# Optimization experiments

Measured on AMD Instinct MI355X. Metric: run time of the kernel, lower is better.

## Reference

```python
import jax, jax.numpy as jnp
import numpy as np

DIM = 768
NUM_HEADS = 12
HEAD_DIM = DIM // NUM_HEADS
SCALE = HEAD_DIM ** -0.5


def setup_inputs() -> dict:
    key = jax.random.key(0)
    ks = jax.random.split(key, 7)
    B, N, C = 8, 1024, DIM
    x = jax.random.normal(ks[0], (B, N, C), dtype=jnp.float32)
    mask = jax.random.randint(ks[1], (B, N), 0, 2) > 0  # True = masked out
    qkv_w = jax.random.normal(ks[2], (3 * C, C), dtype=jnp.float32) * 0.02
    q_bias = jax.random.normal(ks[3], (C,), dtype=jnp.float32) * 0.02
    v_bias = jax.random.normal(ks[4], (C,), dtype=jnp.float32) * 0.02
    proj_w = jax.random.normal(ks[5], (C, C), dtype=jnp.float32) * 0.02
    proj_b = jax.random.normal(ks[6], (C,), dtype=jnp.float32) * 0.02
    return {"x": x, "mask": mask, "qkv_w": qkv_w, "q_bias": q_bias,
            "v_bias": v_bias, "proj_w": proj_w, "proj_b": proj_b}


def reference(x, mask, qkv_w, q_bias, v_bias, proj_w, proj_b):
    B, N, C = x.shape
    # CAE bias: concat(q_bias, zeros, v_bias) for the fused qkv projection
    qkv_bias = jnp.concatenate([q_bias, jnp.zeros_like(v_bias), v_bias])
    qkv = x @ qkv_w.T + qkv_bias  # [B, N, 3C]
    qkv = qkv.reshape(B, N, 3, NUM_HEADS, HEAD_DIM)
    q, k, v = (qkv[:, :, i].transpose(0, 2, 1, 3) for i in range(3))  # [B,H,N,hd]
    attn = jnp.einsum('bhqd,bhkd->bhqk', q * SCALE, k)  # [B,H,N,N]
    attn = jnp.where(mask[:, None, None, :], -jnp.inf, attn)
    attn = jax.nn.softmax(attn, axis=-1)
    out = jnp.einsum('bhqk,bhkd->bhqd', attn, v)  # [B,H,N,hd]
    out = out.transpose(0, 2, 1, 3).reshape(B, N, C)
    return out @ proj_w.T + proj_b
```

## Files before the change

### kernel.cpp

```cpp
#include <hip/hip_runtime.h>
#include <cstddef>
#include <cstdint>


typedef __attribute__((ext_vector_type(4))) float f32x4;
typedef __attribute__((ext_vector_type(8))) __bf16 bf16x8;
typedef __attribute__((ext_vector_type(4))) unsigned int uint4v;
typedef __attribute__((ext_vector_type(2))) unsigned int uint2v;
typedef __attribute__((ext_vector_type(4))) unsigned short ushort4v;

#define QK_PRESCALE 0.18033688011112042f

__device__ __forceinline__ unsigned short f2bf(float f) {
  return (unsigned short)((__float_as_uint(f) + 0x8000u) >> 16);
}
__device__ __forceinline__ unsigned int pack2bf(float flo, float fhi) {
  unsigned ulo = __float_as_uint(flo) + 0x8000u;
  unsigned uhi = __float_as_uint(fhi) + 0x8000u;
  return __builtin_amdgcn_perm(uhi, ulo, 0x07060302);
}

__device__ __forceinline__ void gl_lds16(const unsigned short* g, unsigned short* l) {
  __builtin_amdgcn_global_load_lds(
      (const __attribute__((address_space(1))) unsigned int*)g,
      (__attribute__((address_space(3))) unsigned int*)l, 16, 0, 0);
}

__global__ __launch_bounds__(256)
void cvt_kernel(const float* __restrict__ src, unsigned short* __restrict__ dst, int n4) {
  int i = blockIdx.x * 256 + threadIdx.x;
  if (i < n4) {
    float4 v = ((const float4*)src)[i];
    uint2v o;
    o.x = pack2bf(v.x, v.y);
    o.y = pack2bf(v.z, v.w);
    ((uint2v*)dst)[i] = o;
  }
}

__global__ __launch_bounds__(256)
void qkv_gemm(const unsigned short* __restrict__ xb, const unsigned short* __restrict__ wb,
              const float* __restrict__ qb, const float* __restrict__ vb,
              unsigned short* __restrict__ qo, unsigned short* __restrict__ ko,
              unsigned short* __restrict__ vto) {
  __shared__ __align__(16) unsigned short smem[17408];
  const int tid = threadIdx.x;
  const int lane = tid & 63, wid = tid >> 6;
  const int lm = lane & 15, lq = lane >> 4;
  const int wm = (wid & 1) * 64, wn = (wid >> 1) * 64;
  const int xsw = lm & 7;
  const int L = blockIdx.x;
  const int xcd = L & 7, s = L >> 3;
  const int m0 = (xcd * 8 + (s & 7)) * 128;
  const int n0 = (s >> 3) * 128;
  const bool sw = (n0 < 1536);
  const unsigned short* Ab = sw ? wb : xb;
  const unsigned short* Bb = sw ? xb : wb;
  const int Ao = sw ? n0 : m0;
  const int Bo = sw ? m0 : n0;
  const int srow = lane >> 3;
  const int scolsw = ((lane & 7) ^ srow) * 8;
  const unsigned short* ga = Ab + (size_t)(Ao + wid * 32 + srow) * 768 + scolsw;
  const unsigned short* gb = Bb + (size_t)(Bo + wid * 32 + srow) * 768 + scolsw;
  f32x4 acc[4][4] = {};

  for (int kt = 0; kt < 768; kt += 64) {
#pragma unroll
    for (int i = 0; i < 4; ++i) {
      gl_lds16(ga + kt + (size_t)i * 8 * 768, &smem[(wid * 32 + i * 8) * 64]);
      gl_lds16(gb + kt + (size_t)i * 8 * 768, &smem[8192 + (wid * 32 + i * 8) * 64]);
    }
    __syncthreads();
#pragma unroll
    for (int ks = 0; ks < 2; ++ks) {
      bf16x8 af[4], bf[4];
#pragma unroll
      for (int i = 0; i < 4; ++i)
        af[i] = *(const bf16x8*)&smem[(wm + i * 16 + lm) * 64 + (((ks * 4 + lq) ^ xsw) * 8)];
#pragma unroll
      for (int i = 0; i < 4; ++i)
        bf[i] = *(const bf16x8*)&smem[8192 + (wn + i * 16 + lm) * 64 + (((ks * 4 + lq) ^ xsw) * 8)];
#pragma unroll
      for (int mi = 0; mi < 4; ++mi)
#pragma unroll
        for (int ni = 0; ni < 4; ++ni)
          acc[mi][ni] = __builtin_amdgcn_mfma_f32_16x16x32_bf16(af[mi], bf[ni], acc[mi][ni], 0, 0, 0);
    }
    __syncthreads();
  }

  if (sw) {
    const int which = (n0 >= 768) ? 1 : 0;
    const int within0 = n0 - which * 768;
#pragma unroll
    for (int mi = 0; mi < 4; ++mi) {
      int d0 = wm + mi * 16 + lq * 4;
      f32x4 bias4 = {0.f, 0.f, 0.f, 0.f};
      if (which == 0) bias4 = *(const f32x4*)&qb[within0 + d0];
#pragma unroll
      for (int ni = 0; ni < 4; ++ni) {
        int tokl = wn + ni * 16 + lm;
        uint2v pk;
        if (which == 0) {
          pk.x = pack2bf((acc[mi][ni][0] + bias4[0]) * QK_PRESCALE,
                         (acc[mi][ni][1] + bias4[1]) * QK_PRESCALE);
          pk.y = pack2bf((acc[mi][ni][2] + bias4[2]) * QK_PRESCALE,
                         (acc[mi][ni][3] + bias4[3]) * QK_PRESCALE);
        } else {
          pk.x = pack2bf(acc[mi][ni][0], acc[mi][ni][1]);
          pk.y = pack2bf(acc[mi][ni][2], acc[mi][ni][3]);
        }
        *(uint2v*)&smem[tokl * 136 + d0] = pk;
      }
    }
    __syncthreads();
    {
      int tok = tid >> 1, half = tid & 1;
      int b = m0 >> 10;
      int tokg = (m0 & 1023) + tok;
      int hh = (within0 >> 6) + half;
      unsigned short* dst = which ? ko : qo;
      size_t base = (((size_t)(b * 12 + hh)) * 1024 + tokg) * 64;
      const unsigned short* srcr = &smem[tok * 136 + half * 64];
#pragma unroll
      for (int j = 0; j < 8; ++j)
        *(uint4v*)&dst[base + j * 8] = *(const uint4v*)&srcr[j * 8];
    }
  } else {
    const int within0 = n0 - 1536;
#pragma unroll
    for (int mi = 0; mi < 4; ++mi) {
      int tok0 = wm + mi * 16 + lq * 4;
#pragma unroll
      for (int ni = 0; ni < 4; ++ni) {
        int dl = wn + ni * 16 + lm;
        float bias = vb[within0 + dl];
        uint2v pk;
        pk.x = pack2bf(acc[mi][ni][0] + bias, acc[mi][ni][1] + bias);
        pk.y = pack2bf(acc[mi][ni][2] + bias, acc[mi][ni][3] + bias);
        *(uint2v*)&smem[dl * 136 + tok0] = pk;
      }
    }
    __syncthreads();
    {
      int dl = tid >> 1, halft = tid & 1;
      int within = within0 + dl;
      int hh = within >> 6, d = within & 63;
      int b = m0 >> 10;
      int tokg0 = (m0 & 1023) + halft * 64;
      size_t base = (((size_t)(b * 12 + hh)) * 64 + d) * 1024 + tokg0;
      const unsigned short* srcr = &smem[dl * 136 + halft * 64];
#pragma unroll
      for (int j = 0; j < 8; ++j)
        *(uint4v*)&vto[base + j * 8] = *(const uint4v*)&srcr[j * 8];
    }
  }
}

__global__ __launch_bounds__(256)
void attn_mfma(const unsigned short* __restrict__ q, const unsigned short* __restrict__ k,
               const unsigned short* __restrict__ vt, const int* __restrict__ mask,
               unsigned short* __restrict__ ao) {
  __shared__ unsigned short ks_s[64 * 64];
  __shared__ unsigned short vs_s[64 * 64];
  __shared__ unsigned short ps[4][32 * 72];
  __shared__ float mkl[64];
  const int tid = threadIdx.x;
  const int lane = tid & 63, wid = tid >> 6;
  const int lm = lane & 15, lq = lane >> 4;
  const int xsw = lm & 7;
  const int L = blockIdx.x;
  const int xcd = L & 7, s = L >> 3;
  const int bh = xcd * 12 + s / 8;
  const int qt = s % 8;
  const int bb = bh / 12, hh = bh % 12;
  const unsigned short* qp = q + (size_t)bh * 65536;
  const unsigned short* kp = k + (size_t)bh * 65536;
  const unsigned short* vp = vt + (size_t)bh * 65536;
  const int* mp = mask + bb * 1024;
  const int q0 = qt * 128 + wid * 32;
  const int srow = lane >> 3;
  const int scolsw = ((lane & 7) ^ srow) * 8;
  const unsigned short* gk = kp + (size_t)(wid * 16 + srow) * 64 + scolsw;
  const unsigned short* gv = vp + (size_t)(wid * 16 + srow) * 1024 + scolsw;

  bf16x8 qf[2][2];
#pragma unroll
  for (int mi = 0; mi < 2; ++mi)
#pragma unroll
    for (int ks2 = 0; ks2 < 2; ++ks2)
      qf[mi][ks2] = *(const bf16x8*)&qp[(size_t)(q0 + mi * 16 + lm) * 64 + ks2 * 32 + lq * 8];
  bf16x8 ones;
#pragma unroll
  for (int i = 0; i < 8; ++i) ones[i] = (__bf16)1.0f;

  f32x4 o_acc[2][4] = {};
  f32x4 l_acc[2] = {};

  for (int kt = 0; kt < 16; ++kt) {
    __syncthreads();
#pragma unroll
    for (int i = 0; i < 2; ++i) {
      gl_lds16(gk + (size_t)kt * 4096 + (size_t)i * 8 * 64, &ks_s[(wid * 16 + i * 8) * 64]);
      gl_lds16(gv + (size_t)kt * 64 + (size_t)i * 8 * 1024, &vs_s[(wid * 16 + i * 8) * 64]);
    }
    if (tid < 64) mkl[tid] = mp[kt * 64 + tid] ? -1e30f : 0.0f;
    __syncthreads();

    f32x4 st[4][2] = {};
#pragma unroll
    for (int ks2 = 0; ks2 < 2; ++ks2) {
      bf16x8 kf[4];
#pragma unroll
      for (int nt = 0; nt < 4; ++nt)
        kf[nt] = *(const bf16x8*)&ks_s[(nt * 16 + lm) * 64 + (((ks2 * 4 + lq) ^ xsw) * 8)];
#pragma unroll
      for (int nt = 0; nt < 4; ++nt)
#pragma unroll
        for (int mi = 0; mi < 2; ++mi)
          st[nt][mi] = __builtin_amdgcn_mfma_f32_16x16x32_bf16(kf[nt], qf[mi][ks2], st[nt][mi], 0, 0, 0);
    }

#pragma unroll
    for (int nt = 0; nt < 4; ++nt) {
      f32x4 mv4 = *(const f32x4*)&mkl[nt * 16 + lq * 4];
#pragma unroll
      for (int mi = 0; mi < 2; ++mi) {
        uint2v pk;
        pk.x = pack2bf(__builtin_amdgcn_exp2f(st[nt][mi][0] + mv4[0]),
                       __builtin_amdgcn_exp2f(st[nt][mi][1] + mv4[1]));
        pk.y = pack2bf(__builtin_amdgcn_exp2f(st[nt][mi][2] + mv4[2]),
                       __builtin_amdgcn_exp2f(st[nt][mi][3] + mv4[3]));
        *(uint2v*)&ps[wid][(mi * 16 + lm) * 72 + nt * 16 + lq * 4] = pk;
      }
    }

#pragma unroll
    for (int ks2 = 0; ks2 < 2; ++ks2) {
      bf16x8 pf[2], vf[4];
#pragma unroll
      for (int mi = 0; mi < 2; ++mi)
        pf[mi] = *(const bf16x8*)&ps[wid][(mi * 16 + lm) * 72 + ks2 * 32 + lq * 8];
#pragma unroll
      for (int nt = 0; nt < 4; ++nt)
        vf[nt] = *(const bf16x8*)&vs_s[(nt * 16 + lm) * 64 + (((ks2 * 4 + lq) ^ xsw) * 8)];
#pragma unroll
      for (int mi = 0; mi < 2; ++mi) {
#pragma unroll
        for (int nt = 0; nt < 4; ++nt)
          o_acc[mi][nt] = __builtin_amdgcn_mfma_f32_16x16x32_bf16(pf[mi], vf[nt], o_acc[mi][nt], 0, 0, 0);
        l_acc[mi] = __builtin_amdgcn_mfma_f32_16x16x32_bf16(pf[mi], ones, l_acc[mi], 0, 0, 0);
      }
    }
  }

#pragma unroll
  for (int mi = 0; mi < 2; ++mi) {
#pragma unroll
    for (int r = 0; r < 4; ++r) {
      float inv = 1.0f / l_acc[mi][r];
      int tok = q0 + mi * 16 + lq * 4 + r;
#pragma unroll
      for (int nt = 0; nt < 4; ++nt)
        ao[(size_t)(bb * 1024 + tok) * 768 + hh * 64 + nt * 16 + lm] = f2bf(o_acc[mi][nt][r] * inv);
    }
  }
}

__global__ __launch_bounds__(256)
void proj_gemm(const unsigned short* __restrict__ ab, const unsigned short* __restrict__ wb,
               const float* __restrict__ pb, float* __restrict__ out) {
  __shared__ unsigned short as[128 * 64];
  __shared__ unsigned short bs[128 * 64];
  const int tid = threadIdx.x;
  const int lane = tid & 63, wid = tid >> 6;
  const int lm = lane & 15, lq = lane >> 4;
  const int xsw = lm & 7;
  const int wm = (wid & 1) * 64, wn = (wid >> 1) * 64;
  const int L = blockIdx.x;
  const int xcd = L & 7, s = L >> 3;
  const int m0 = (xcd * 8 + s / 6) * 128;
  const int n0 = (s % 6) * 128;
  const int srow = lane >> 3;
  const int scolsw = ((lane & 7) ^ srow) * 8;
  const unsigned short* ga = wb + (size_t)(n0 + wid * 32 + srow) * 768 + scolsw;
  const unsigned short* gb = ab + (size_t)(m0 + wid * 32 + srow) * 768 + scolsw;
  f32x4 acc[4][4] = {};
  for (int kt = 0; kt < 768; kt += 64) {
#pragma unroll
    for (int i = 0; i < 4; ++i) {
      gl_lds16(ga + kt + (size_t)i * 8 * 768, &as[(wid * 32 + i * 8) * 64]);
      gl_lds16(gb + kt + (size_t)i * 8 * 768, &bs[(wid * 32 + i * 8) * 64]);
    }
    __syncthreads();
#pragma unroll
    for (int ks = 0; ks < 2; ++ks) {
      bf16x8 af[4], bf[4];
#pragma unroll
      for (int i = 0; i < 4; ++i)
        af[i] = *(const bf16x8*)&as[(wm + i * 16 + lm) * 64 + (((ks * 4 + lq) ^ xsw) * 8)];
#pragma unroll
      for (int i = 0; i < 4; ++i)
        bf[i] = *(const bf16x8*)&bs[(wn + i * 16 + lm) * 64 + (((ks * 4 + lq) ^ xsw) * 8)];
#pragma unroll
      for (int mi = 0; mi < 4; ++mi)
#pragma unroll
        for (int ni = 0; ni < 4; ++ni)
          acc[mi][ni] = __builtin_amdgcn_mfma_f32_16x16x32_bf16(af[mi], bf[ni], acc[mi][ni], 0, 0, 0);
    }
    __syncthreads();
  }
#pragma unroll
  for (int mi = 0; mi < 4; ++mi) {
    int gn0 = n0 + wm + mi * 16 + lq * 4;
    f32x4 bias4 = *(const f32x4*)&pb[gn0];
#pragma unroll
    for (int ni = 0; ni < 4; ++ni) {
      int gm = m0 + wn + ni * 16 + lm;
      f32x4 o;
      o[0] = acc[mi][ni][0] + bias4[0];
      o[1] = acc[mi][ni][1] + bias4[1];
      o[2] = acc[mi][ni][2] + bias4[2];
      o[3] = acc[mi][ni][3] + bias4[3];
      *(f32x4*)&out[(size_t)gm * 768 + gn0] = o;
    }
  }
}

extern "C" void kernel_launch(void* const* d_in, const int* in_sizes, int n_in,
                              void* d_out, int out_size, void* d_ws, size_t ws_size,
                              hipStream_t stream) {
  const float* x      = (const float*)d_in[0];
  const int*   mask   = (const int*)d_in[1];
  const float* qkv_w  = (const float*)d_in[2];
  const float* q_bias = (const float*)d_in[3];
  const float* v_bias = (const float*)d_in[4];
  const float* proj_w = (const float*)d_in[5];
  const float* proj_b = (const float*)d_in[6];
  float* out = (float*)d_out;
  unsigned short* p = (unsigned short*)d_ws;
  unsigned short* xb     = p;              p += 6291456;
  unsigned short* wqkvb  = p;              p += 1769472;
  unsigned short* wprojb = p;              p += 589824;
  unsigned short* qo     = p;              p += 6291456;
  unsigned short* ko     = p;              p += 6291456;
  unsigned short* vto    = p;              p += 6291456;
  unsigned short* ao     = p;

  cvt_kernel<<<6144, 256, 0, stream>>>(x, xb, 1572864);
  cvt_kernel<<<1728, 256, 0, stream>>>(qkv_w, wqkvb, 442368);
  cvt_kernel<<<576, 256, 0, stream>>>(proj_w, wprojb, 147456);
  qkv_gemm<<<1152, 256, 0, stream>>>(xb, wqkvb, q_bias, v_bias, qo, ko, vto);
  attn_mfma<<<768, 256, 0, stream>>>(qo, ko, vto, mask, ao);
  proj_gemm<<<384, 256, 0, stream>>>(ao, wprojb, proj_b, out);
}
```

Measured before the change: 204.9 us.

## Rewrite QKV GEMM as 256x256 double-buffered pipelined tile and fuse conversions

```diff
diff --git a/kernel.cpp b/kernel.cpp
--- a/kernel.cpp
+++ b/kernel.cpp
@@ -7,7 +7,6 @@
 typedef __attribute__((ext_vector_type(8))) __bf16 bf16x8;
 typedef __attribute__((ext_vector_type(4))) unsigned int uint4v;
 typedef __attribute__((ext_vector_type(2))) unsigned int uint2v;
-typedef __attribute__((ext_vector_type(4))) unsigned short ushort4v;
 
 #define QK_PRESCALE 0.18033688011112042f
 
@@ -27,81 +26,132 @@
 }
 
 __global__ __launch_bounds__(256)
-void cvt_kernel(const float* __restrict__ src, unsigned short* __restrict__ dst, int n4) {
-  int i = blockIdx.x * 256 + threadIdx.x;
+void cvt3_kernel(const float* __restrict__ s0, unsigned short* __restrict__ d0,
+                 const float* __restrict__ s1, unsigned short* __restrict__ d1,
+                 const float* __restrict__ s2, unsigned short* __restrict__ d2) {
+  int bid = blockIdx.x;
+  const float* s; unsigned short* d; int i; int n4;
+  if (bid < 6144)      { s = s0; d = d0; i = bid * 256 + threadIdx.x;            n4 = 1572864; }
+  else if (bid < 7872) { s = s1; d = d1; i = (bid - 6144) * 256 + threadIdx.x;   n4 = 442368; }
+  else                 { s = s2; d = d2; i = (bid - 7872) * 256 + threadIdx.x;   n4 = 147456; }
   if (i < n4) {
-    float4 v = ((const float4*)src)[i];
+    float4 v = ((const float4*)s)[i];
     uint2v o;
     o.x = pack2bf(v.x, v.y);
     o.y = pack2bf(v.z, v.w);
-    ((uint2v*)dst)[i] = o;
-  }
-}
-
-__global__ __launch_bounds__(256)
+    ((uint2v*)d)[i] = o;
+  }
+}
+
+__global__ __launch_bounds__(512, 2)
 void qkv_gemm(const unsigned short* __restrict__ xb, const unsigned short* __restrict__ wb,
               const float* __restrict__ qb, const float* __restrict__ vb,
               unsigned short* __restrict__ qo, unsigned short* __restrict__ ko,
               unsigned short* __restrict__ vto) {
-  __shared__ __align__(16) unsigned short smem[17408];
+  __shared__ __align__(16) unsigned short lds[65536];
   const int tid = threadIdx.x;
   const int lane = tid & 63, wid = tid >> 6;
   const int lm = lane & 15, lq = lane >> 4;
-  const int wm = (wid & 1) * 64, wn = (wid >> 1) * 64;
   const int xsw = lm & 7;
+  const int wr = wid >> 2, wc = wid & 3;
   const int L = blockIdx.x;
   const int xcd = L & 7, s = L >> 3;
-  const int m0 = (xcd * 8 + (s & 7)) * 128;
-  const int n0 = (s >> 3) * 128;
-  const bool sw = (n0 < 1536);
-  const unsigned short* Ab = sw ? wb : xb;
-  const unsigned short* Bb = sw ? xb : wb;
-  const int Ao = sw ? n0 : m0;
-  const int Bo = sw ? m0 : n0;
+  const int tt = xcd * 4 + s / 9;
+  const int ft = s % 9;
+  const int m0 = tt * 256;
+  const int n0 = ft * 256;
   const int srow = lane >> 3;
   const int scolsw = ((lane & 7) ^ srow) * 8;
-  const unsigned short* ga = Ab + (size_t)(Ao + wid * 32 + srow) * 768 + scolsw;
-  const unsigned short* gb = Bb + (size_t)(Bo + wid * 32 + srow) * 768 + scolsw;
-  f32x4 acc[4][4] = {};
-
-  for (int kt = 0; kt < 768; kt += 64) {
-#pragma unroll
-    for (int i = 0; i < 4; ++i) {
-      gl_lds16(ga + kt + (size_t)i * 8 * 768, &smem[(wid * 32 + i * 8) * 64]);
-      gl_lds16(gb + kt + (size_t)i * 8 * 768, &smem[8192 + (wid * 32 + i * 8) * 64]);
-    }
-    __syncthreads();
-#pragma unroll
-    for (int ks = 0; ks < 2; ++ks) {
-      bf16x8 af[4], bf[4];
-#pragma unroll
-      for (int i = 0; i < 4; ++i)
-        af[i] = *(const bf16x8*)&smem[(wm + i * 16 + lm) * 64 + (((ks * 4 + lq) ^ xsw) * 8)];
-#pragma unroll
-      for (int i = 0; i < 4; ++i)
-        bf[i] = *(const bf16x8*)&smem[8192 + (wn + i * 16 + lm) * 64 + (((ks * 4 + lq) ^ xsw) * 8)];
-#pragma unroll
-      for (int mi = 0; mi < 4; ++mi)
-#pragma unroll
-        for (int ni = 0; ni < 4; ++ni)
-          acc[mi][ni] = __builtin_amdgcn_mfma_f32_16x16x32_bf16(af[mi], bf[ni], acc[mi][ni], 0, 0, 0);
-    }
-    __syncthreads();
-  }
-
-  if (sw) {
-    const int which = (n0 >= 768) ? 1 : 0;
-    const int within0 = n0 - which * 768;
-#pragma unroll
-    for (int mi = 0; mi < 4; ++mi) {
-      int d0 = wm + mi * 16 + lq * 4;
+  const int laG = wr * 128 + wc * 16;
+  const int lbG = (wid >> 1) * 64 + (wid & 1) * 16;
+  const unsigned short* pa = wb + (size_t)(n0 + laG + srow) * 768 + scolsw;
+  const unsigned short* pb = xb + (size_t)(m0 + lbG + srow) * 768 + scolsw;
+
+  f32x4 acc[8][4] = {};
+
+#define STAGE_A(g, tgt) { \
+    const unsigned short* _s = pa + (size_t)(g) * 64 * 768 + (size_t)(tgt) * 64; \
+    unsigned short* _d = &lds[(((tgt) & 1) * 256 + laG + (g) * 64) * 64]; \
+    gl_lds16(_s, _d); \
+    gl_lds16(_s + (size_t)8 * 768, _d + 8 * 64); }
+
+#define STAGE_B(g, tgt) { \
+    const unsigned short* _s = pb + (size_t)(g) * 32 * 768 + (size_t)(tgt) * 64; \
+    unsigned short* _d = &lds[32768 + (((tgt) & 1) * 256 + lbG + (g) * 32) * 64]; \
+    gl_lds16(_s, _d); \
+    gl_lds16(_s + (size_t)8 * 768, _d + 8 * 64); }
+
+#define PHASE_COMPUTE(qA, qB, bufb) { \
+    const unsigned short* _Ab = &lds[(bufb) * 16384]; \
+    const unsigned short* _Bb = &lds[32768 + (bufb) * 16384]; \
+    bf16x8 af[4][2], bff[2][2]; \
+    _Pragma("unroll") for (int m2 = 0; m2 < 4; ++m2) \
+      _Pragma("unroll") for (int kx = 0; kx < 2; ++kx) \
+        af[m2][kx] = *(const bf16x8*)&_Ab[(wr * 128 + ((qA) * 4 + m2) * 16 + lm) * 64 + (((kx * 4 + lq) ^ xsw) * 8)]; \
+    _Pragma("unroll") for (int n2 = 0; n2 < 2; ++n2) \
+      _Pragma("unroll") for (int kx = 0; kx < 2; ++kx) \
+        bff[n2][kx] = *(const bf16x8*)&_Bb[(wc * 64 + ((qB) * 2 + n2) * 16 + lm) * 64 + (((kx * 4 + lq) ^ xsw) * 8)]; \
+    __builtin_amdgcn_s_setprio(1); \
+    _Pragma("unroll") for (int kx = 0; kx < 2; ++kx) \
+      _Pragma("unroll") for (int m2 = 0; m2 < 4; ++m2) \
+        _Pragma("unroll") for (int n2 = 0; n2 < 2; ++n2) \
+          acc[(qA) * 4 + m2][(qB) * 2 + n2] = __builtin_amdgcn_mfma_f32_16x16x32_bf16( \
+              af[m2][kx], bff[n2][kx], acc[(qA) * 4 + m2][(qB) * 2 + n2], 0, 0, 0); \
+    __builtin_amdgcn_s_setprio(0); }
+
+#define BAR_A_VM10() asm volatile("s_waitcnt vmcnt(10)\ns_barrier" ::: "memory")
+#define BAR_A_VM8()  asm volatile("s_waitcnt vmcnt(8)\ns_barrier" ::: "memory")
+#define BAR_A()      asm volatile("s_barrier" ::: "memory")
+#define BAR_B()      asm volatile("s_waitcnt lgkmcnt(0)\ns_barrier" ::: "memory")
+
+  STAGE_A(0, 0); STAGE_B(0, 0); STAGE_A(1, 0); STAGE_B(1, 0);
+  STAGE_A(0, 1); STAGE_B(0, 1);
+
+  for (int t = 0; t < 12; ++t) {
+    const int b = t & 1;
+    const int t1c = (t + 1 < 12) ? t + 1 : 11;
+    const int t2c = (t + 2 < 12) ? t + 2 : 11;
+    STAGE_A(1, t1c);
+    BAR_A_VM10();
+    PHASE_COMPUTE(0, 0, b);
+    BAR_B();
+    STAGE_B(1, t1c);
+    BAR_A_VM8();
+    PHASE_COMPUTE(0, 1, b);
+    BAR_B();
+    STAGE_A(0, t2c);
+    BAR_A();
+    PHASE_COMPUTE(1, 0, b);
+    BAR_B();
+    STAGE_B(0, t2c);
+    BAR_A();
+    PHASE_COMPUTE(1, 1, b);
+    BAR_B();
+  }
+  asm volatile("s_waitcnt vmcnt(0)" ::: "memory");
+
+#undef STAGE_A
+#undef STAGE_B
+#undef PHASE_COMPUTE
+
+  const int bq = tt >> 2;
+  const int tokb = (tt & 3) * 256;
+  if (ft < 6) {
+    const bool isq = ft < 3;
+    unsigned short* dst0 = isq ? qo : ko;
+    const int fbase = (isq ? ft : ft - 3) * 256 + wr * 128;
+#pragma unroll
+    for (int mi = 0; mi < 8; ++mi) {
+      const int dg = fbase + mi * 16 + lq * 4;
+      const int hh = dg >> 6;
+      const int dih = dg & 63;
       f32x4 bias4 = {0.f, 0.f, 0.f, 0.f};
-      if (which == 0) bias4 = *(const f32x4*)&qb[within0 + d0];
+      if (isq) bias4 = *(const f32x4*)&qb[ft * 256 + wr * 128 + mi * 16 + lq * 4];
 #pragma unroll
       for (int ni = 0; ni < 4; ++ni) {
-        int tokl = wn + ni * 16 + lm;
+        const int tok = tokb + wc * 64 + ni * 16 + lm;
         uint2v pk;
-        if (which == 0) {
+        if (isq) {
           pk.x = pack2bf((acc[mi][ni][0] + bias4[0]) * QK_PRESCALE,
                          (acc[mi][ni][1] + bias4[1]) * QK_PRESCALE);
           pk.y = pack2bf((acc[mi][ni][2] + bias4[2]) * QK_PRESCALE,
@@ -110,49 +160,39 @@
           pk.x = pack2bf(acc[mi][ni][0], acc[mi][ni][1]);
           pk.y = pack2bf(acc[mi][ni][2], acc[mi][ni][3]);
         }
-        *(uint2v*)&smem[tokl * 136 + d0] = pk;
-      }
-    }
-    __syncthreads();
-    {
-      int tok = tid >> 1, half = tid & 1;
-      int b = m0 >> 10;
-      int tokg = (m0 & 1023) + tok;
-      int hh = (within0 >> 6) + half;
-      unsigned short* dst = which ? ko : qo;
-      size_t base = (((size_t)(b * 12 + hh)) * 1024 + tokg) * 64;
-      const unsigned short* srcr = &smem[tok * 136 + half * 64];
-#pragma unroll
-      for (int j = 0; j < 8; ++j)
-        *(uint4v*)&dst[base + j * 8] = *(const uint4v*)&srcr[j * 8];
+        *(uint2v*)&dst0[(((size_t)(bq * 12 + hh)) * 1024 + tok) * 64 + dih] = pk;
+      }
     }
   } else {
-    const int within0 = n0 - 1536;
-#pragma unroll
-    for (int mi = 0; mi < 4; ++mi) {
-      int tok0 = wm + mi * 16 + lq * 4;
-#pragma unroll
-      for (int ni = 0; ni < 4; ++ni) {
-        int dl = wn + ni * 16 + lm;
-        float bias = vb[within0 + dl];
-        uint2v pk;
-        pk.x = pack2bf(acc[mi][ni][0] + bias, acc[mi][ni][1] + bias);
-        pk.y = pack2bf(acc[mi][ni][2] + bias, acc[mi][ni][3] + bias);
-        *(uint2v*)&smem[dl * 136 + tok0] = pk;
-      }
-    }
-    __syncthreads();
-    {
-      int dl = tid >> 1, halft = tid & 1;
-      int within = within0 + dl;
-      int hh = within >> 6, d = within & 63;
-      int b = m0 >> 10;
-      int tokg0 = (m0 & 1023) + halft * 64;
-      size_t base = (((size_t)(b * 12 + hh)) * 64 + d) * 1024 + tokg0;
-      const unsigned short* srcr = &smem[dl * 136 + halft * 64];
-#pragma unroll
-      for (int j = 0; j < 8; ++j)
-        *(uint4v*)&vto[base + j * 8] = *(const uint4v*)&srcr[j * 8];
+    const int vb0 = (ft - 6) * 256;
+    unsigned short* scr = lds;
+#pragma unroll
+    for (int p = 0; p < 2; ++p) {
+      __syncthreads();
+      if (wr == p) {
+#pragma unroll
+        for (int mi = 0; mi < 8; ++mi) {
+          f32x4 bias4 = *(const f32x4*)&vb[vb0 + p * 128 + mi * 16 + lq * 4];
+#pragma unroll
+          for (int ni = 0; ni < 4; ++ni) {
+            const int tok = wc * 64 + ni * 16 + lm;
+#pragma unroll
+            for (int r = 0; r < 4; ++r)
+              scr[(mi * 16 + lq * 4 + r) * 264 + tok] = f2bf(acc[mi][ni][r] + bias4[r]);
+          }
+        }
+      }
+      __syncthreads();
+      {
+        const int row = tid >> 2, tq = tid & 3;
+        const int dgv = vb0 + p * 128 + row;
+        const int hh = dgv >> 6, d = dgv & 63;
+        unsigned short* dstv = vto + (((size_t)(bq * 12 + hh)) * 64 + d) * 1024 + tokb + tq * 64;
+        const unsigned short* srcr = &scr[row * 264 + tq * 64];
+#pragma unroll
+        for (int j = 0; j < 8; ++j)
+          *(uint4v*)&dstv[j * 8] = *(const uint4v*)&srcr[j * 8];
+      }
     }
   }
 }
@@ -347,10 +387,8 @@
   unsigned short* vto    = p;              p += 6291456;
   unsigned short* ao     = p;
 
-  cvt_kernel<<<6144, 256, 0, stream>>>(x, xb, 1572864);
-  cvt_kernel<<<1728, 256, 0, stream>>>(qkv_w, wqkvb, 442368);
-  cvt_kernel<<<576, 256, 0, stream>>>(proj_w, wprojb, 147456);
-  qkv_gemm<<<1152, 256, 0, stream>>>(xb, wqkvb, q_bias, v_bias, qo, ko, vto);
+  cvt3_kernel<<<8448, 256, 0, stream>>>(x, xb, qkv_w, wqkvb, proj_w, wprojb);
+  qkv_gemm<<<288, 512, 0, stream>>>(xb, wqkvb, q_bias, v_bias, qo, ko, vto);
   attn_mfma<<<768, 256, 0, stream>>>(qo, ko, vto, mask, ao);
   proj_gemm<<<384, 256, 0, stream>>>(ao, wprojb, proj_b, out);
 }
```

New measurement: 205.1 us. Within noise of the previous version (+0.1%).
